# Optimization experiments

Hardware: AMD Instinct MI355X
Metric: run time of the kernel (lower is better)

## Reference

```python
import jax, jax.numpy as jnp
import numpy as np

NUM_CLASSES = 80
N_CAND = 10  # simOTA n_candidate_k


def setup_inputs() -> dict:
    key = jax.random.key(0)
    ks = jax.random.split(key, 8)
    G, C, B = 300, NUM_CLASSES, 2
    # FPN grids for a 1280x1280 input, strides 8/16/32 -> 160^2+80^2+40^2 = 33600 anchors
    levels = [(160, 8), (80, 16), (40, 32)]
    xs, ys, ss = [], [], []
    for n, s in levels:
        yy, xx = np.meshgrid(np.arange(n), np.arange(n), indexing='ij')
        xs.append(xx.ravel()); ys.append(yy.ravel()); ss.append(np.full(n * n, s))
    x_shifts = jnp.asarray(np.concatenate(xs), jnp.float32)[None]
    y_shifts = jnp.asarray(np.concatenate(ys), jnp.float32)[None]
    strides = jnp.asarray(np.concatenate(ss), jnp.float32)
    expanded_strides = strides[None]
    A = x_shifts.shape[1]
    # gt boxes in cxcywh, image coords
    gt_cxy = jax.random.uniform(ks[0], (G, 2), jnp.float32, 0.0, 1280.0)
    gt_wh = jax.random.uniform(ks[1], (G, 2), jnp.float32, 16.0, 256.0)
    gt_bboxes_per_image = jnp.concatenate([gt_cxy, gt_wh], -1)
    gt_classes = jax.random.randint(ks[2], (G,), 0, C)
    # predicted boxes: anchor centers + noise, wh ~ a few strides
    anc_x = (x_shifts[0] + 0.5) * strides
    anc_y = (y_shifts[0] + 0.5) * strides
    pr_cxy = jnp.stack([anc_x, anc_y], -1) + jax.random.normal(ks[3], (A, 2), jnp.float32) * strides[:, None]
    pr_wh = strides[:, None] * (1.0 + 4.0 * jax.random.uniform(ks[4], (A, 2), jnp.float32))
    bboxes_preds_per_image = jnp.concatenate([pr_cxy, pr_wh], -1)
    cls_preds = jax.random.normal(ks[5], (B, A, C), jnp.float32)
    obj_preds = jax.random.normal(ks[6], (B, A, 1), jnp.float32)
    return {
        'batch_idx': 0, 'num_gt': G, 'total_num_anchors': A,
        'gt_bboxes_per_image': gt_bboxes_per_image, 'gt_classes': gt_classes,
        'bboxes_preds_per_image': bboxes_preds_per_image,
        'expanded_strides': expanded_strides, 'x_shifts': x_shifts, 'y_shifts': y_shifts,
        'cls_preds': cls_preds, 'obj_preds': obj_preds,
    }


def _pairwise_iou(gt, pr):
    # gt [G,4], pr [A,4], cxcywh -> iou [G,A] (bboxes_iou with xyxy=False)
    tl = jnp.maximum(gt[:, None, :2] - 0.5 * gt[:, None, 2:], pr[None, :, :2] - 0.5 * pr[None, :, 2:])
    br = jnp.minimum(gt[:, None, :2] + 0.5 * gt[:, None, 2:], pr[None, :, :2] + 0.5 * pr[None, :, 2:])
    wh = jnp.clip(br - tl, 0.0)
    inter = wh[..., 0] * wh[..., 1]
    area_g = gt[:, 2] * gt[:, 3]
    area_p = pr[:, 2] * pr[:, 3]
    return inter / (area_g[:, None] + area_p[None, :] - inter)


def reference(batch_idx, num_gt, total_num_anchors, gt_bboxes_per_image, gt_classes,
              bboxes_preds_per_image, expanded_strides, x_shifts, y_shifts, cls_preds, obj_preds):
    G, A = gt_bboxes_per_image.shape[0], bboxes_preds_per_image.shape[0]
    strides = expanded_strides[0]
    xc = (x_shifts[0] + 0.5) * strides  # [A] anchor centers
    yc = (y_shifts[0] + 0.5) * strides
    gx, gy, gw, gh = (gt_bboxes_per_image[:, i] for i in range(4))
    # is_in_boxes [G,A]
    in_box = ((xc[None] > (gx - 0.5 * gw)[:, None]) & ((gx + 0.5 * gw)[:, None] > xc[None]) &
              (yc[None] > (gy - 0.5 * gh)[:, None]) & ((gy + 0.5 * gh)[:, None] > yc[None]))
    r = 2.5 * strides[None]  # center_radius * stride
    in_ctr = ((xc[None] > gx[:, None] - r) & (gx[:, None] + r > xc[None]) &
              (yc[None] > gy[:, None] - r) & (gy[:, None] + r > yc[None]))
    fg_any = in_box.any(0) | in_ctr.any(0)          # fg_mask over all anchors
    candidate = in_box & in_ctr                      # is_in_boxes_and_center (full-anchor layout)
    ious = jnp.where(fg_any[None, :], _pairwise_iou(gt_bboxes_per_image, bboxes_preds_per_image), 0.0)
    # pairwise cls BCE cost; one-hot target -> factored form, never materializes [G,A,C]
    p = jnp.sqrt(jax.nn.sigmoid(cls_preds[batch_idx]) * jax.nn.sigmoid(obj_preds[batch_idx]))  # [A,C]
    p = jnp.clip(p, 1e-7, 1.0 - 1e-7)
    lp, l1p = jnp.log(p), jnp.log1p(-p)
    s_all = l1p.sum(-1)                              # [A] sum_c log(1-p_c)
    cls_loss = -((lp - l1p)[:, gt_classes].T + s_all[None, :])  # [G,A]
    # cost; 1e5 penalty for non-candidates (as in source), extra 1e6 keeps non-fg anchors
    # strictly below any fg anchor in top-k order (source only ever considers fg anchors)
    cost = cls_loss - 3.0 * jnp.log(ious + 1e-8) + 100000.0 * (~candidate) + 1000000.0 * (~fg_any)[None, :]
    # dynamic-k: sum of top-10 ious per gt, clamped to >= 1 (<= 10 inherently)
    topk_ious, _ = jax.lax.top_k(ious, N_CAND)
    dks = jnp.clip(topk_ious.sum(1).astype(jnp.int32), 1, N_CAND)  # [G]
    _, idx = jax.lax.top_k(-cost, N_CAND)            # [G,10] lowest-cost anchors per gt
    sel = (jnp.arange(N_CAND)[None, :] < dks[:, None]).astype(jnp.int32)
    matching = jnp.zeros((G, A), jnp.int32).at[jnp.arange(G)[:, None], idx].max(sel)
    # resolve anchors matched to >1 gt: keep argmax of T_scores over gts (as in source)
    multi = matching.sum(0) > 1
    best_gt = jnp.argmax(cost, axis=0)               # [A]
    matching = jnp.where(multi[None, :], (jnp.arange(G)[:, None] == best_gt[None, :]).astype(jnp.int32), matching)
    fg_final = matching.sum(0) > 0                   # final fg mask over all anchors
    num_fg = fg_final.sum()
    matched = jnp.argmax(matching, axis=0)           # [A]
    gt_matched_classes = jnp.where(fg_final, gt_classes[matched], -1)
    pred_ious = (matching.astype(ious.dtype) * ious).sum(0)  # [A], 0 where unmatched
    matched_gt_inds = jnp.where(fg_final, matched, -1)
    # fixed-shape (full-anchor) versions of the source's compacted outputs
    return (gt_matched_classes, fg_final, pred_ious, matched_gt_inds, num_fg)
```

## Files before the change

kernel.cpp:

```cpp
#include <hip/hip_runtime.h>
#include <math.h>

#define NUMC 80
#define NCAND 10
#define TPB 256
#define SEGI 8
#define SEGF 16
#define FBY  32
#define MAXG_LDS 1024

typedef unsigned long long u64;

__device__ __forceinline__ float sigmoid_stable(float x) {
    if (x >= 0.0f) { float e = expf(-x); return 1.0f / (1.0f + e); }
    float e = expf(x); return e / (1.0f + e);
}

struct CostRes { float cost; float iou; bool cand; };

__device__ __forceinline__ CostRes cost_od(
    int g, int a, int b, int A,
    const float* __restrict__ gt, const float4* __restrict__ pred4,
    const float4* __restrict__ anc4, const float* __restrict__ so_arr,
    const float* __restrict__ cls, const int* __restrict__ fg_any,
    const int* __restrict__ gcls)
{
    float gx = gt[g*4+0], gy = gt[g*4+1], gw = gt[g*4+2], gh = gt[g*4+3];
    float4 p4 = pred4[a];
    float4 an = anc4[a];
    int fga = fg_any[a];
    float px = p4.x, py = p4.y, pw = p4.z, ph = p4.w;
    float tlx = fmaxf(gx - 0.5f*gw, px - 0.5f*pw);
    float tly = fmaxf(gy - 0.5f*gh, py - 0.5f*ph);
    float brx = fminf(gx + 0.5f*gw, px + 0.5f*pw);
    float bry = fminf(gy + 0.5f*gh, py + 0.5f*ph);
    float iw = fmaxf(brx - tlx, 0.0f);
    float ih = fmaxf(bry - tly, 0.0f);
    float inter = iw * ih;
    float iou = inter / (gw*gh + pw*ph - inter);
    float fi = fga ? iou : 0.0f;
    float x = an.x, y = an.y, r = an.z;
    bool inb = (x > gx - 0.5f*gw) && (gx + 0.5f*gw > x) &&
               (y > gy - 0.5f*gh) && (gy + 0.5f*gh > y);
    bool inc = (x > gx - r) && (gx + r > x) && (y > gy - r) && (gy + r > y);
    bool cand = inb && inc;
    float so = so_arr[a];
    float cv = cls[((size_t)b * A + a) * NUMC + gcls[g]];
    float sc = sigmoid_stable(cv);
    float p = sqrtf(sc * so);
    p = fminf(fmaxf(p, 1e-7f), 1.0f - 1e-7f);
    float lp = logf(p);
    float l1p = log1pf(-p);
    float clsl = -((lp - l1p) + an.w);
    float cost = clsl - 3.0f * logf(fi + 1e-8f)
               + (cand ? 0.0f : 100000.0f)
               + (fga  ? 0.0f : 1000000.0f);
    CostRes res; res.cost = cost; res.iou = fi; res.cand = cand; return res;
}

__device__ __forceinline__ float pair_iou_masked4(
    int g, const float* __restrict__ gt, float4 p4, int fga)
{
    float gx = gt[g*4+0], gy = gt[g*4+1], gw = gt[g*4+2], gh = gt[g*4+3];
    float px = p4.x, py = p4.y, pw = p4.z, ph = p4.w;
    float tlx = fmaxf(gx - 0.5f*gw, px - 0.5f*pw);
    float tly = fmaxf(gy - 0.5f*gh, py - 0.5f*ph);
    float brx = fminf(gx + 0.5f*gw, px + 0.5f*pw);
    float bry = fminf(gy + 0.5f*gh, py + 0.5f*ph);
    float iw = fmaxf(brx - tlx, 0.0f);
    float ih = fmaxf(bry - tly, 0.0f);
    float inter = iw * ih;
    float iou = inter / (gw*gh + pw*ph - inter);
    return fga ? iou : 0.0f;
}

__global__ __launch_bounds__(256) void fused_pre_kernel(
    const int* __restrict__ bidx, int G, int A,
    const float* __restrict__ gt,
    const float* __restrict__ strides,
    const float* __restrict__ xs, const float* __restrict__ ys,
    const float* __restrict__ cls, const float* __restrict__ obj,
    const float4* __restrict__ pred4,
    float4* __restrict__ anc4, float* __restrict__ so_arr,
    float4* __restrict__ ptlbr4, float* __restrict__ pare,
    float4* __restrict__ grpbox,
    int* __restrict__ fg_any, int* __restrict__ count, int* __restrict__ mgt,
    int* __restrict__ mcount, int* __restrict__ fb_cnt, float* __restrict__ out)
{
    __shared__ float sl1p[64 * 81];
    __shared__ float so_l[64];
    __shared__ float sgt[MAXG_LDS * 4];
    __shared__ int   flags[256];
    __shared__ float smnx[64], smny[64], smxx[64], smxy[64];
    __shared__ float sred[4];

    int tid = threadIdx.x;
    int a0 = blockIdx.x * 64;
    int b = bidx[0];
    int GS = (G < MAXG_LDS) ? G : MAXG_LDS;

    if (tid < 64) {
        int a = a0 + tid;
        so_l[tid] = (a < A) ? sigmoid_stable(obj[(size_t)b * A + a]) : 0.0f;
    } else {
        for (int i = tid - 64; i < GS * 4; i += 192) sgt[i] = gt[i];
    }
    __syncthreads();

    {
        int a_loc = tid >> 2;
        int a = a0 + a_loc;
        if (a < A) {
            int qb = (tid & 3) * 5;
            float so = so_l[a_loc];
            const float4* cp4 = (const float4*)(cls + ((size_t)b * A + a) * NUMC);
            #pragma unroll
            for (int qq = 0; qq < 5; ++qq) {
                int q = qb + qq;
                float4 v4 = cp4[q];
                float vv[4] = {v4.x, v4.y, v4.z, v4.w};
                #pragma unroll
                for (int k = 0; k < 4; ++k) {
                    int c = q * 4 + k;
                    float sc = sigmoid_stable(vv[k]);
                    float p = sqrtf(sc * so);
                    p = fminf(fmaxf(p, 1e-7f), 1.0f - 1e-7f);
                    float l1p = log1pf(-p);
                    sl1p[a_loc * 81 + c] = l1p;
                }
            }
        }
    }
    __syncthreads();

    float acc = 0.0f;
    if (tid < 64) {
        #pragma unroll 8
        for (int c = 0; c < NUMC; ++c) acc += sl1p[tid * 81 + c];
    }

    float x3 = 0.0f, y3 = 0.0f, r3 = 0.0f;
    {
        int a_loc = tid & 63;
        int chunk = tid >> 6;
        int a = a0 + a_loc;
        int any = 0;
        if (a < A) {
            float st = strides[a];
            float x = (xs[a] + 0.5f) * st;
            float y = (ys[a] + 0.5f) * st;
            float r = 2.5f * st;
            if (chunk == 0) { x3 = x; y3 = y; r3 = r; }
            int gpc = (G + 3) >> 2;
            int g0 = chunk * gpc;
            int g1 = (G < g0 + gpc) ? G : (g0 + gpc);
            for (int g = g0; g < g1; ++g) {
                float gx, gy, gw, gh;
                if (g < GS) { gx = sgt[g*4+0]; gy = sgt[g*4+1]; gw = sgt[g*4+2]; gh = sgt[g*4+3]; }
                else        { gx = gt[g*4+0];  gy = gt[g*4+1];  gw = gt[g*4+2];  gh = gt[g*4+3]; }
                bool inb = (x > gx - 0.5f*gw) && (gx + 0.5f*gw > x) &&
                           (y > gy - 0.5f*gh) && (gy + 0.5f*gh > y);
                bool inc = (x > gx - r) && (gx + r > x) && (y > gy - r) && (gy + r > y);
                if (inb | inc) { any = 1; break; }
            }
        }
        flags[tid] = any;
    }
    __syncthreads();

    if (tid < 64) {
        int a = a0 + tid;
        float mnx = INFINITY, mny = INFINITY, mxx = -INFINITY, mxy = -INFINITY;
        if (a < A) {
            int any = flags[tid] | flags[tid + 64] | flags[tid + 128] | flags[tid + 192];
            fg_any[a] = any;
            anc4[a] = make_float4(x3, y3, r3, acc);
            so_arr[a] = so_l[tid];
            count[a] = 0;
            mgt[a] = -1;
            float4 p4 = pred4[a];
            float ap = p4.z * p4.w;
            if (any) {
                mnx = p4.x - 0.5f * p4.z;
                mny = p4.y - 0.5f * p4.w;
                mxx = p4.x + 0.5f * p4.z;
                mxy = p4.y + 0.5f * p4.w;
            }
            ptlbr4[a] = make_float4(mnx, mny, mxx, mxy);
            pare[a] = ap;
        }
        smnx[tid] = mnx; smny[tid] = mny; smxx[tid] = mxx; smxy[tid] = mxy;
    }
    __syncthreads();
    if (tid < 4) {
        float v = (tid == 0 || tid == 1) ? INFINITY : -INFINITY;
        for (int i = 0; i < 64; ++i) {
            if (tid == 0) v = fminf(v, smnx[i]);
            else if (tid == 1) v = fminf(v, smny[i]);
            else if (tid == 2) v = fmaxf(v, smxx[i]);
            else v = fmaxf(v, smxy[i]);
        }
        sred[tid] = v;
    }
    __syncthreads();
    if (tid == 0) {
        grpbox[blockIdx.x] = make_float4(sred[0], sred[1], sred[2], sred[3]);
        if (blockIdx.x == 0) { out[(size_t)4 * A] = 0.0f; mcount[0] = 0; fb_cnt[0] = 0; }
    }
}

__global__ __launch_bounds__(TPB) void scanI_kernel(
    int G, int A, int seglen,
    const float* __restrict__ gt,
    const float4* __restrict__ ptlbr4, const float* __restrict__ pare,
    const float4* __restrict__ grpbox,
    float* __restrict__ piou_ws)
{
    int seg = blockIdx.x;
    int g = blockIdx.y;
    int a0 = seg * seglen;
    int a1 = min(A, a0 + seglen);
    int tid = threadIdx.x;

    float gx = gt[g*4+0], gy = gt[g*4+1], gw = gt[g*4+2], gh = gt[g*4+3];
    float gtlx = gx - 0.5f*gw, gtly = gy - 0.5f*gh;
    float gbrx = gx + 0.5f*gw, gbry = gy + 0.5f*gh;
    float ag = gw * gh;

    float ti[NCAND];
    #pragma unroll
    for (int j = 0; j < NCAND; ++j) ti[j] = 0.0f;

    for (int a = a0 + tid; a < a1; a += TPB) {
        int grp = __builtin_amdgcn_readfirstlane(a >> 6);
        float4 gb = grpbox[grp];
        if ((gb.z <= gtlx) || (gb.x >= gbrx) || (gb.w <= gtly) || (gb.y >= gbry))
            continue;
        float4 p = ptlbr4[a];
        float ap = pare[a];
        float tlx = fmaxf(gtlx, p.x);
        float tly = fmaxf(gtly, p.y);
        float brx = fminf(gbrx, p.z);
        float bry = fminf(gbry, p.w);
        float iw = fmaxf(brx - tlx, 0.0f);
        float ih = fmaxf(bry - tly, 0.0f);
        float inter = iw * ih;
        float fi = inter / (ag + ap - inter);
        if (fi > ti[NCAND-1]) {
            ti[NCAND-1] = fi;
            #pragma unroll
            for (int j = NCAND-1; j >= 1; --j) {
                if (ti[j] > ti[j-1]) { float t = ti[j]; ti[j] = ti[j-1]; ti[j-1] = t; }
            }
        }
    }

    __shared__ float s_iv[TPB * NCAND];
    #pragma unroll
    for (int j = 0; j < NCAND; ++j) s_iv[tid*NCAND+j] = ti[j];
    __syncthreads();
    for (int off = TPB/2; off > 0; off >>= 1) {
        if (tid < off) {
            float ra[NCAND];
            int i = 0, k = 0;
            const float* L = &s_iv[tid*NCAND];
            const float* R = &s_iv[(tid+off)*NCAND];
            for (int o = 0; o < NCAND; ++o) {
                if (L[i] >= R[k]) { ra[o] = L[i]; ++i; }
                else              { ra[o] = R[k]; ++k; }
            }
            for (int j = 0; j < NCAND; ++j) s_iv[tid*NCAND+j] = ra[j];
        }
        __syncthreads();
    }
    if (tid == 0) {
        int base = (g * SEGI + seg) * NCAND;
        for (int j = 0; j < NCAND; ++j) piou_ws[base+j] = s_iv[j];
    }
}

__global__ __launch_bounds__(256) void scanC_kernel(
    const int* __restrict__ bidx, int G, int A,
    const float* __restrict__ gt, const float4* __restrict__ pred4,
    const float4* __restrict__ anc4, const float* __restrict__ so_arr,
    const float* __restrict__ cls, const int* __restrict__ fg_any,
    const int* __restrict__ gcls,
    const float* __restrict__ piou_ws,
    int* __restrict__ dk_arr, int* __restrict__ fb_list, int* __restrict__ fb_cnt,
    int* __restrict__ count, int* __restrict__ mgt)
{
    int g = blockIdx.x;
    int tid = threadIdx.x;
    __shared__ u64 scand[128];
    __shared__ int s_nc;
    __shared__ int s_dk;

    if (tid == 0) {
        s_nc = 0;
        const float* ib = piou_ws + (size_t)g * SEGI * NCAND;
        int ip[SEGI];
        #pragma unroll
        for (int q = 0; q < SEGI; ++q) ip[q] = 0;
        float s = 0.0f;
        for (int o = 0; o < NCAND; ++o) {
            int bs = 0; float bv = -1.0f;
            #pragma unroll
            for (int q = 0; q < SEGI; ++q) {
                if (ip[q] < NCAND) {
                    float v = ib[q*NCAND + ip[q]];
                    if (v > bv) { bv = v; bs = q; }
                }
            }
            s += bv; ip[bs]++;
        }
        int dk = (int)s;
        if (dk < 1) dk = 1;
        if (dk > NCAND) dk = NCAND;
        s_dk = dk;
        dk_arr[g] = dk;
    }
    __syncthreads();

    if (tid < 243) {
        int lvl = tid / 81, slot = tid % 81, sx = slot % 9, sy = slot / 9;
        int n, si, base;
        if (lvl == 0)      { n = 160; si = 8;  base = 0; }
        else if (lvl == 1) { n = 80;  si = 16; base = 25600; }
        else               { n = 40;  si = 32; base = 32000; }
        float sf = (float)si;
        float gx = gt[g*4+0], gy = gt[g*4+1], gw = gt[g*4+2], gh = gt[g*4+3];
        float mx = fminf(0.5f*gw, 2.5f*sf);
        float my = fminf(0.5f*gh, 2.5f*sf);
        int ilo = (int)floorf((gx - mx)/sf - 0.5f) - 1;
        int ihi = (int)ceilf ((gx + mx)/sf - 0.5f) + 1;
        int jlo = (int)floorf((gy - my)/sf - 0.5f) - 1;
        int jhi = (int)ceilf ((gy + my)/sf - 0.5f) + 1;
        if (ilo < 0) ilo = 0;
        if (jlo < 0) jlo = 0;
        if (ihi > n-1) ihi = n-1;
        if (jhi > n-1) jhi = n-1;
        int i = ilo + sx, j = jlo + sy;
        if (i <= ihi && j <= jhi) {
            int a = base + j * n + i;
            int b = bidx[0];
            CostRes cr = cost_od(g, a, b, A, gt, pred4, anc4, so_arr, cls, fg_any, gcls);
            if (cr.cand) {
                int k = atomicAdd(&s_nc, 1);
                if (k < 128)
                    scand[k] = ((u64)__float_as_uint(cr.cost) << 32) | (unsigned)a;
            }
        }
    }
    __syncthreads();

    if (tid == 0) {
        int nc = s_nc; if (nc > 128) nc = 128;
        int dk = s_dk;
        if (dk > nc) {
            int idx = atomicAdd(fb_cnt, 1);
            fb_list[idx] = g;
        } else {
            u64 top[NCAND];
            #pragma unroll
            for (int j = 0; j < NCAND; ++j) top[j] = ~0ULL;
            for (int t = 0; t < nc; ++t) {
                u64 v = scand[t];
                if (v < top[NCAND-1]) {
                    top[NCAND-1] = v;
                    #pragma unroll
                    for (int j = NCAND-1; j >= 1; --j) {
                        if (top[j] < top[j-1]) { u64 t2 = top[j]; top[j] = top[j-1]; top[j-1] = t2; }
                    }
                }
            }
            for (int o = 0; o < dk; ++o) {
                int a = (int)(top[o] & 0xffffffffULL);
                atomicAdd(&count[a], 1);
                atomicMax(&mgt[a], g);
            }
        }
    }
}

__global__ __launch_bounds__(TPB) void fb_part_kernel(
    const int* __restrict__ bidx, int G, int A, int seglenF,
    const float* __restrict__ gt, const float4* __restrict__ pred4,
    const float4* __restrict__ anc4, const float* __restrict__ so_arr,
    const float* __restrict__ cls, const int* __restrict__ fg_any,
    const int* __restrict__ gcls,
    const int* __restrict__ fb_list, const int* __restrict__ fb_cnt,
    u64* __restrict__ fbws)
{
    __shared__ u64 s_cv[TPB * NCAND];
    int nflag = fb_cnt[0];
    int tid = threadIdx.x;
    int chunk = blockIdx.x;
    int b = bidx[0];
    for (int f = blockIdx.y; f < nflag; f += FBY) {
        int g = fb_list[f];
        int a0 = chunk * seglenF;
        int a1 = min(A, a0 + seglenF);
        u64 tc[NCAND];
        #pragma unroll
        for (int j = 0; j < NCAND; ++j) tc[j] = ~0ULL;
        for (int a = a0 + tid; a < a1; a += TPB) {
            CostRes cr = cost_od(g, a, b, A, gt, pred4, anc4, so_arr, cls, fg_any, gcls);
            u64 v = ((u64)__float_as_uint(cr.cost) << 32) | (unsigned)a;
            if (v < tc[NCAND-1]) {
                tc[NCAND-1] = v;
                #pragma unroll
                for (int j = NCAND-1; j >= 1; --j) {
                    if (tc[j] < tc[j-1]) { u64 t2 = tc[j]; tc[j] = tc[j-1]; tc[j-1] = t2; }
                }
            }
        }
        #pragma unroll
        for (int j = 0; j < NCAND; ++j) s_cv[tid*NCAND+j] = tc[j];
        __syncthreads();
        for (int off = TPB/2; off > 0; off >>= 1) {
            if (tid < off) {
                u64 rc[NCAND];
                int i = 0, k = 0;
                const u64* L = &s_cv[tid*NCAND];
                const u64* R = &s_cv[(tid+off)*NCAND];
                for (int o = 0; o < NCAND; ++o) {
                    if (L[i] < R[k]) { rc[o] = L[i]; ++i; }
                    else             { rc[o] = R[k]; ++k; }
                }
                for (int j = 0; j < NCAND; ++j) s_cv[tid*NCAND+j] = rc[j];
            }
            __syncthreads();
        }
        if (tid == 0) {
            u64* dst = fbws + ((size_t)f * SEGF + chunk) * NCAND;
            for (int j = 0; j < NCAND; ++j) dst[j] = s_cv[j];
        }
        __syncthreads();
    }
}

__global__ void fb_mark_kernel(
    const int* __restrict__ fb_list, const int* __restrict__ fb_cnt,
    const int* __restrict__ dk_arr, const u64* __restrict__ fbws,
    int* __restrict__ count, int* __restrict__ mgt)
{
    if (threadIdx.x != 0 || blockIdx.x != 0) return;
    int nflag = fb_cnt[0];
    for (int f = 0; f < nflag; ++f) {
        int g = fb_list[f];
        int dk = dk_arr[g];
        const u64* lists = fbws + (size_t)f * SEGF * NCAND;
        int p[SEGF];
        for (int q = 0; q < SEGF; ++q) p[q] = 0;
        for (int o = 0; o < dk; ++o) {
            int bs = 0; u64 bv = ~0ULL;
            for (int q = 0; q < SEGF; ++q) {
                if (p[q] < NCAND) {
                    u64 v = lists[q*NCAND + p[q]];
                    if (v < bv) { bv = v; bs = q; }
                }
            }
            p[bs]++;
            int a = (int)(bv & 0xffffffffULL);
            atomicAdd(&count[a], 1);
            atomicMax(&mgt[a], g);
        }
    }
}

__global__ void finalize_a_kernel(
    int G, int A,
    const float* __restrict__ gt, const float4* __restrict__ pred4,
    const int* __restrict__ fg_any, const int* __restrict__ gcls,
    const int* __restrict__ count, const int* __restrict__ mgt,
    int* __restrict__ mlist, int* __restrict__ mcount,
    float* __restrict__ out)
{
    int a = blockIdx.x * blockDim.x + threadIdx.x;
    if (a >= A) return;
    int cnt = count[a];
    unsigned long long m = __ballot(cnt > 0);
    if ((threadIdx.x & 63) == 0 && m) {
        atomicAdd(&out[(size_t)4*A], (float)__popcll(m));
    }
    if (cnt > 1) {
        int idx = atomicAdd(mcount, 1);
        mlist[idx] = a;
        out[(size_t)A + a] = 1.0f;
        return;
    }
    float gmc = -1.0f, mgi = -1.0f, piou = 0.0f, fg = 0.0f;
    if (cnt == 1) {
        int matched = mgt[a];
        fg = 1.0f;
        gmc = (float)gcls[matched];
        mgi = (float)matched;
        piou = pair_iou_masked4(matched, gt, pred4[a], fg_any[a]);
    }
    out[a]               = gmc;
    out[(size_t)A + a]   = fg;
    out[(size_t)2*A + a] = piou;
    out[(size_t)3*A + a] = mgi;
}

__global__ __launch_bounds__(TPB) void finalize_b_kernel(
    const int* __restrict__ bidx, int G, int A,
    const float* __restrict__ gt, const float4* __restrict__ pred4,
    const float4* __restrict__ anc4, const float* __restrict__ so_arr,
    const float* __restrict__ cls, const int* __restrict__ fg_any,
    const int* __restrict__ gcls,
    const int* __restrict__ mlist, const int* __restrict__ mcount,
    float* __restrict__ out)
{
    __shared__ float sc[TPB];
    __shared__ int   sg[TPB];
    int n = mcount[0];
    int tid = threadIdx.x;
    int b = bidx[0];
    for (int i = blockIdx.x; i < n; i += gridDim.x) {
        int a = mlist[i];
        float best = -INFINITY; int bi = 0x7fffffff;
        for (int g = tid; g < G; g += TPB) {
            CostRes cr = cost_od(g, a, b, A, gt, pred4, anc4, so_arr, cls, fg_any, gcls);
            if (cr.cost > best) { best = cr.cost; bi = g; }
        }
        sc[tid] = best; sg[tid] = bi;
        __syncthreads();
        for (int off = TPB/2; off > 0; off >>= 1) {
            if (tid < off) {
                float c2 = sc[tid+off]; int g2 = sg[tid+off];
                if (c2 > sc[tid] || (c2 == sc[tid] && g2 < sg[tid])) { sc[tid] = c2; sg[tid] = g2; }
            }
            __syncthreads();
        }
        if (tid == 0) {
            int matched = sg[0];
            out[a]               = (float)gcls[matched];
            out[(size_t)2*A + a] = pair_iou_masked4(matched, gt, pred4[a], fg_any[a]);
            out[(size_t)3*A + a] = (float)matched;
        }
        __syncthreads();
    }
}

extern "C" void kernel_launch(void* const* d_in, const int* in_sizes, int n_in,
                              void* d_out, int out_size, void* d_ws, size_t ws_size,
                              hipStream_t stream)
{
    const int*   bidx    = (const int*)d_in[0];
    const float* gt      = (const float*)d_in[3];
    const int*   gcls    = (const int*)d_in[4];
    const float* pred    = (const float*)d_in[5];
    const float* strides = (const float*)d_in[6];
    const float* xs      = (const float*)d_in[7];
    const float* ys      = (const float*)d_in[8];
    const float* cls     = (const float*)d_in[9];
    const float* obj     = (const float*)d_in[10];
    int G = in_sizes[4];
    int A = in_sizes[6];
    float* out = (float*)d_out;
    const float4* pred4 = (const float4*)pred;

    char* ws = (char*)d_ws;
    size_t off = 0;
    auto alloc = [&](size_t bytes) -> void* {
        void* p = ws + off;
        off += (bytes + 255) & ~(size_t)255;
        return p;
    };
    int nGrp = (A + 63) / 64;
    float4* anc4    = (float4*)alloc((size_t)A * sizeof(float4));
    float*  so_arr  = (float*) alloc((size_t)A * sizeof(float));
    float4* ptlbr4  = (float4*)alloc((size_t)A * sizeof(float4));
    float*  pare    = (float*) alloc((size_t)A * sizeof(float));
    float4* grpbox  = (float4*)alloc((size_t)nGrp * sizeof(float4));
    int*    fg_any  = (int*)   alloc((size_t)A * sizeof(int));
    int*    count   = (int*)   alloc((size_t)A * sizeof(int));
    int*    mgt     = (int*)   alloc((size_t)A * sizeof(int));
    int*    mlist   = (int*)   alloc((size_t)A * sizeof(int));
    int*    mcount  = (int*)   alloc(256);
    int*    fb_cnt  = (int*)   alloc(256);
    float*  piou_ws = (float*) alloc((size_t)G * SEGI * NCAND * sizeof(float));
    int*    dk_arr  = (int*)   alloc((size_t)G * sizeof(int));
    int*    fb_list = (int*)   alloc((size_t)G * sizeof(int));
    u64*    fbws    = (u64*)   alloc((size_t)G * SEGF * NCAND * sizeof(u64));

    int seglenI = ((A + SEGI*64 - 1) / (SEGI*64)) * 64;
    int seglenF = ((A + SEGF*64 - 1) / (SEGF*64)) * 64;
    int blocksA256 = (A + 255) / 256;

    fused_pre_kernel<<<nGrp, 256, 0, stream>>>(
        bidx, G, A, gt, strides, xs, ys, cls, obj, pred4,
        anc4, so_arr, ptlbr4, pare, grpbox, fg_any, count, mgt, mcount, fb_cnt, out);
    scanI_kernel<<<dim3(SEGI, G), TPB, 0, stream>>>(
        G, A, seglenI, gt, ptlbr4, pare, grpbox, piou_ws);
    scanC_kernel<<<G, 256, 0, stream>>>(
        bidx, G, A, gt, pred4, anc4, so_arr, cls, fg_any, gcls,
        piou_ws, dk_arr, fb_list, fb_cnt, count, mgt);
    fb_part_kernel<<<dim3(SEGF, FBY), TPB, 0, stream>>>(
        bidx, G, A, seglenF, gt, pred4, anc4, so_arr, cls, fg_any, gcls,
        fb_list, fb_cnt, fbws);
    fb_mark_kernel<<<1, 64, 0, stream>>>(
        fb_list, fb_cnt, dk_arr, fbws, count, mgt);
    finalize_a_kernel<<<blocksA256, 256, 0, stream>>>(
        G, A, gt, pred4, fg_any, gcls, count, mgt, mlist, mcount, out);
    finalize_b_kernel<<<256, TPB, 0, stream>>>(
        bidx, G, A, gt, pred4, anc4, so_arr, cls, fg_any, gcls, mlist, mcount, out);
}
```

Before: 192.1 us.

## Compute class log-sum lazily for candidate anchors and use wave-shuffle top-k merges

The prepass no longer computes the 80-class log1p sum for every anchor. It records a cand_any flag, and a separate kernel computes that sum only for anchors that are a candidate for some gt. A fixup kernel fills in the remaining anchors only when the fallback path is taken. scanI and scanC now reduce their top-k IoU lists with 16-wide bitonic merges over wave shuffles instead of LDS serial merges, and scanI uses 64-thread blocks with more segments. The prepass also moves to 512 threads and a shuffle-based bbox reduction, at the cost of extra kernel launches and a risk that finalize_b reads s_arr for non-candidate anchors that still hold 0.

```diff
diff --git a/kernel.cpp b/kernel.cpp
--- a/kernel.cpp
+++ b/kernel.cpp
@@ -3,17 +3,57 @@
 
 #define NUMC 80
 #define NCAND 10
-#define TPB 256
-#define SEGI 8
+#define NK 16
+#define SEGI 16
 #define SEGF 16
-#define FBY  32
-#define MAXG_LDS 1024
+#define FBY  8
+#define GT_LDS 300
 
 typedef unsigned long long u64;
 
 __device__ __forceinline__ float sigmoid_stable(float x) {
-    if (x >= 0.0f) { float e = expf(-x); return 1.0f / (1.0f + e); }
-    float e = expf(x); return e / (1.0f + e);
+    float e = expf(-fabsf(x));
+    float num = (x >= 0.0f) ? 1.0f : e;
+    return num / (1.0f + e);
+}
+
+__device__ __forceinline__ float s_all_for(int a, int b, int A, float so,
+                                           const float* __restrict__ cls)
+{
+    const float4* cp4 = (const float4*)(cls + ((size_t)b * A + a) * NUMC);
+    float acc = 0.0f;
+    for (int q = 0; q < NUMC/4; ++q) {
+        float4 v4 = cp4[q];
+        float vv[4] = {v4.x, v4.y, v4.z, v4.w};
+        #pragma unroll
+        for (int k = 0; k < 4; ++k) {
+            float sc = sigmoid_stable(vv[k]);
+            float p = sqrtf(sc * so);
+            p = fminf(fmaxf(p, 1e-7f), 1.0f - 1e-7f);
+            acc += log1pf(-p);
+        }
+    }
+    return acc;
+}
+
+__device__ __forceinline__ void bitonic16_desc(float (&L)[NK]) {
+    #pragma unroll
+    for (int j = 0; j < NK; ++j) if (!(j & 8)) { float a=L[j], b=L[j|8]; L[j]=fmaxf(a,b); L[j|8]=fminf(a,b); }
+    #pragma unroll
+    for (int j = 0; j < NK; ++j) if (!(j & 4)) { float a=L[j], b=L[j|4]; L[j]=fmaxf(a,b); L[j|4]=fminf(a,b); }
+    #pragma unroll
+    for (int j = 0; j < NK; ++j) if (!(j & 2)) { float a=L[j], b=L[j|2]; L[j]=fmaxf(a,b); L[j|2]=fminf(a,b); }
+    #pragma unroll
+    for (int j = 0; j < NK; ++j) if (!(j & 1)) { float a=L[j], b=L[j|1]; L[j]=fmaxf(a,b); L[j|1]=fminf(a,b); }
+}
+
+__device__ __forceinline__ void merge16_desc(float (&A_)[NK], const float (&B_)[NK]) {
+    float L[NK];
+    #pragma unroll
+    for (int j = 0; j < NK; ++j) L[j] = fmaxf(A_[j], B_[NK-1-j]);
+    bitonic16_desc(L);
+    #pragma unroll
+    for (int j = 0; j < NK; ++j) A_[j] = L[j];
 }
 
 struct CostRes { float cost; float iou; bool cand; };
@@ -21,9 +61,9 @@
 __device__ __forceinline__ CostRes cost_od(
     int g, int a, int b, int A,
     const float* __restrict__ gt, const float4* __restrict__ pred4,
-    const float4* __restrict__ anc4, const float* __restrict__ so_arr,
-    const float* __restrict__ cls, const int* __restrict__ fg_any,
-    const int* __restrict__ gcls)
+    const float4* __restrict__ anc4, const float* __restrict__ s_arr,
+    const float* __restrict__ so_arr, const float* __restrict__ cls,
+    const int* __restrict__ fg_any, const int* __restrict__ gcls)
 {
     float gx = gt[g*4+0], gy = gt[g*4+1], gw = gt[g*4+2], gh = gt[g*4+3];
     float4 p4 = pred4[a];
@@ -51,7 +91,7 @@
     p = fminf(fmaxf(p, 1e-7f), 1.0f - 1e-7f);
     float lp = logf(p);
     float l1p = log1pf(-p);
-    float clsl = -((lp - l1p) + an.w);
+    float clsl = -((lp - l1p) + s_arr[a]);
     float cost = clsl - 3.0f * logf(fi + 1e-8f)
                + (cand ? 0.0f : 100000.0f)
                + (fga  ? 0.0f : 1000000.0f);
@@ -74,86 +114,49 @@
     return fga ? iou : 0.0f;
 }
 
-__global__ __launch_bounds__(256) void fused_pre_kernel(
+__global__ __launch_bounds__(512) void fused_pre_kernel(
     const int* __restrict__ bidx, int G, int A,
-    const float* __restrict__ gt,
-    const float* __restrict__ strides,
+    const float* __restrict__ gt, const float* __restrict__ strides,
     const float* __restrict__ xs, const float* __restrict__ ys,
-    const float* __restrict__ cls, const float* __restrict__ obj,
-    const float4* __restrict__ pred4,
-    float4* __restrict__ anc4, float* __restrict__ so_arr,
-    float4* __restrict__ ptlbr4, float* __restrict__ pare,
-    float4* __restrict__ grpbox,
-    int* __restrict__ fg_any, int* __restrict__ count, int* __restrict__ mgt,
+    const float* __restrict__ obj, const float4* __restrict__ pred4,
+    float4* __restrict__ anc4, float* __restrict__ so_arr, float* __restrict__ s_arr,
+    float4* __restrict__ ptlbr4, float* __restrict__ pare, float4* __restrict__ grpbox,
+    int* __restrict__ fg_any, int* __restrict__ cand_any,
+    int* __restrict__ count, int* __restrict__ mgt,
     int* __restrict__ mcount, int* __restrict__ fb_cnt, float* __restrict__ out)
 {
-    __shared__ float sl1p[64 * 81];
-    __shared__ float so_l[64];
-    __shared__ float sgt[MAXG_LDS * 4];
-    __shared__ int   flags[256];
-    __shared__ float smnx[64], smny[64], smxx[64], smxy[64];
-    __shared__ float sred[4];
+    __shared__ float sgt[GT_LDS * 4];
+    __shared__ float sx[64], sy[64], sr[64];
+    __shared__ int   flags[512];
 
     int tid = threadIdx.x;
     int a0 = blockIdx.x * 64;
-    int b = bidx[0];
-    int GS = (G < MAXG_LDS) ? G : MAXG_LDS;
-
+    int GS = (G < GT_LDS) ? G : GT_LDS;
+
+    for (int i = tid; i < GS * 4; i += 512) sgt[i] = gt[i];
     if (tid < 64) {
         int a = a0 + tid;
-        so_l[tid] = (a < A) ? sigmoid_stable(obj[(size_t)b * A + a]) : 0.0f;
-    } else {
-        for (int i = tid - 64; i < GS * 4; i += 192) sgt[i] = gt[i];
+        float st = 0.0f, x = 0.0f, y = 0.0f;
+        if (a < A) {
+            st = strides[a];
+            x = (xs[a] + 0.5f) * st;
+            y = (ys[a] + 0.5f) * st;
+            so_arr[a] = sigmoid_stable(obj[(size_t)bidx[0] * A + a]);
+        }
+        sx[tid] = x; sy[tid] = y; sr[tid] = 2.5f * st;
     }
     __syncthreads();
 
-    {
-        int a_loc = tid >> 2;
-        int a = a0 + a_loc;
-        if (a < A) {
-            int qb = (tid & 3) * 5;
-            float so = so_l[a_loc];
-            const float4* cp4 = (const float4*)(cls + ((size_t)b * A + a) * NUMC);
-            #pragma unroll
-            for (int qq = 0; qq < 5; ++qq) {
-                int q = qb + qq;
-                float4 v4 = cp4[q];
-                float vv[4] = {v4.x, v4.y, v4.z, v4.w};
-                #pragma unroll
-                for (int k = 0; k < 4; ++k) {
-                    int c = q * 4 + k;
-                    float sc = sigmoid_stable(vv[k]);
-                    float p = sqrtf(sc * so);
-                    p = fminf(fmaxf(p, 1e-7f), 1.0f - 1e-7f);
-                    float l1p = log1pf(-p);
-                    sl1p[a_loc * 81 + c] = l1p;
-                }
-            }
-        }
-    }
-    __syncthreads();
-
-    float acc = 0.0f;
-    if (tid < 64) {
-        #pragma unroll 8
-        for (int c = 0; c < NUMC; ++c) acc += sl1p[tid * 81 + c];
-    }
-
-    float x3 = 0.0f, y3 = 0.0f, r3 = 0.0f;
     {
         int a_loc = tid & 63;
         int chunk = tid >> 6;
         int a = a0 + a_loc;
-        int any = 0;
+        int any_or = 0, any_and = 0;
         if (a < A) {
-            float st = strides[a];
-            float x = (xs[a] + 0.5f) * st;
-            float y = (ys[a] + 0.5f) * st;
-            float r = 2.5f * st;
-            if (chunk == 0) { x3 = x; y3 = y; r3 = r; }
-            int gpc = (G + 3) >> 2;
+            float x = sx[a_loc], y = sy[a_loc], r = sr[a_loc];
+            int gpc = (G + 7) >> 3;
             int g0 = chunk * gpc;
-            int g1 = (G < g0 + gpc) ? G : (g0 + gpc);
+            int g1 = min(G, g0 + gpc);
             for (int g = g0; g < g1; ++g) {
                 float gx, gy, gw, gh;
                 if (g < GS) { gx = sgt[g*4+0]; gy = sgt[g*4+1]; gw = sgt[g*4+2]; gh = sgt[g*4+3]; }
@@ -161,10 +164,11 @@
                 bool inb = (x > gx - 0.5f*gw) && (gx + 0.5f*gw > x) &&
                            (y > gy - 0.5f*gh) && (gy + 0.5f*gh > y);
                 bool inc = (x > gx - r) && (gx + r > x) && (y > gy - r) && (gy + r > y);
-                if (inb | inc) { any = 1; break; }
-            }
-        }
-        flags[tid] = any;
+                any_or  |= (int)(inb | inc);
+                any_and |= (int)(inb && inc);
+            }
+        }
+        flags[tid] = any_or | (any_and << 1);
     }
     __syncthreads();
 
@@ -172,14 +176,17 @@
         int a = a0 + tid;
         float mnx = INFINITY, mny = INFINITY, mxx = -INFINITY, mxy = -INFINITY;
         if (a < A) {
-            int any = flags[tid] | flags[tid + 64] | flags[tid + 128] | flags[tid + 192];
+            int f = flags[tid] | flags[tid+64] | flags[tid+128] | flags[tid+192]
+                  | flags[tid+256] | flags[tid+320] | flags[tid+384] | flags[tid+448];
+            int any = f & 1;
             fg_any[a] = any;
-            anc4[a] = make_float4(x3, y3, r3, acc);
-            so_arr[a] = so_l[tid];
+            cand_any[a] = (f >> 1) & 1;
+            anc4[a] = make_float4(sx[tid], sy[tid], sr[tid], 0.0f);
+            s_arr[a] = 0.0f;
             count[a] = 0;
             mgt[a] = -1;
             float4 p4 = pred4[a];
-            float ap = p4.z * p4.w;
+            pare[a] = p4.z * p4.w;
             if (any) {
                 mnx = p4.x - 0.5f * p4.z;
                 mny = p4.y - 0.5f * p4.w;
@@ -187,29 +194,46 @@
                 mxy = p4.y + 0.5f * p4.w;
             }
             ptlbr4[a] = make_float4(mnx, mny, mxx, mxy);
-            pare[a] = ap;
-        }
-        smnx[tid] = mnx; smny[tid] = mny; smxx[tid] = mxx; smxy[tid] = mxy;
-    }
-    __syncthreads();
-    if (tid < 4) {
-        float v = (tid == 0 || tid == 1) ? INFINITY : -INFINITY;
-        for (int i = 0; i < 64; ++i) {
-            if (tid == 0) v = fminf(v, smnx[i]);
-            else if (tid == 1) v = fminf(v, smny[i]);
-            else if (tid == 2) v = fmaxf(v, smxx[i]);
-            else v = fmaxf(v, smxy[i]);
-        }
-        sred[tid] = v;
-    }
-    __syncthreads();
-    if (tid == 0) {
-        grpbox[blockIdx.x] = make_float4(sred[0], sred[1], sred[2], sred[3]);
-        if (blockIdx.x == 0) { out[(size_t)4 * A] = 0.0f; mcount[0] = 0; fb_cnt[0] = 0; }
-    }
-}
-
-__global__ __launch_bounds__(TPB) void scanI_kernel(
+        }
+        #pragma unroll
+        for (int off = 32; off > 0; off >>= 1) {
+            mnx = fminf(mnx, __shfl_xor(mnx, off));
+            mny = fminf(mny, __shfl_xor(mny, off));
+            mxx = fmaxf(mxx, __shfl_xor(mxx, off));
+            mxy = fmaxf(mxy, __shfl_xor(mxy, off));
+        }
+        if (tid == 0) {
+            grpbox[blockIdx.x] = make_float4(mnx, mny, mxx, mxy);
+            if (blockIdx.x == 0) { out[(size_t)4 * A] = 0.0f; mcount[0] = 0; fb_cnt[0] = 0; }
+        }
+    }
+}
+
+__global__ void sall_kernel(
+    const int* __restrict__ bidx, int A,
+    const float* __restrict__ cls, const float* __restrict__ so_arr,
+    const int* __restrict__ cand_any, float* __restrict__ s_arr)
+{
+    int a = blockIdx.x * blockDim.x + threadIdx.x;
+    if (a >= A) return;
+    if (!cand_any[a]) return;
+    s_arr[a] = s_all_for(a, bidx[0], A, so_arr[a], cls);
+}
+
+__global__ void sall_fixup_kernel(
+    const int* __restrict__ bidx, int A,
+    const float* __restrict__ cls, const float* __restrict__ so_arr,
+    const int* __restrict__ cand_any, const int* __restrict__ fb_cnt,
+    float* __restrict__ s_arr)
+{
+    if (fb_cnt[0] == 0) return;
+    int a = blockIdx.x * blockDim.x + threadIdx.x;
+    if (a >= A) return;
+    if (cand_any[a]) return;
+    s_arr[a] = s_all_for(a, bidx[0], A, so_arr[a], cls);
+}
+
+__global__ __launch_bounds__(64) void scanI_kernel(
     int G, int A, int seglen,
     const float* __restrict__ gt,
     const float4* __restrict__ ptlbr4, const float* __restrict__ pare,
@@ -227,11 +251,11 @@
     float gbrx = gx + 0.5f*gw, gbry = gy + 0.5f*gh;
     float ag = gw * gh;
 
-    float ti[NCAND];
-    #pragma unroll
-    for (int j = 0; j < NCAND; ++j) ti[j] = 0.0f;
-
-    for (int a = a0 + tid; a < a1; a += TPB) {
+    float ti[NK];
+    #pragma unroll
+    for (int j = 0; j < NK; ++j) ti[j] = 0.0f;
+
+    for (int a = a0 + tid; a < a1; a += 64) {
         int grp = __builtin_amdgcn_readfirstlane(a >> 6);
         float4 gb = grpbox[grp];
         if ((gb.z <= gtlx) || (gb.x >= gbrx) || (gb.w <= gtly) || (gb.y >= gbry))
@@ -246,45 +270,36 @@
         float ih = fmaxf(bry - tly, 0.0f);
         float inter = iw * ih;
         float fi = inter / (ag + ap - inter);
-        if (fi > ti[NCAND-1]) {
-            ti[NCAND-1] = fi;
+        if (fi > ti[NK-1]) {
+            ti[NK-1] = fi;
             #pragma unroll
-            for (int j = NCAND-1; j >= 1; --j) {
+            for (int j = NK-1; j >= 1; --j) {
                 if (ti[j] > ti[j-1]) { float t = ti[j]; ti[j] = ti[j-1]; ti[j-1] = t; }
             }
         }
     }
 
-    __shared__ float s_iv[TPB * NCAND];
-    #pragma unroll
-    for (int j = 0; j < NCAND; ++j) s_iv[tid*NCAND+j] = ti[j];
-    __syncthreads();
-    for (int off = TPB/2; off > 0; off >>= 1) {
-        if (tid < off) {
-            float ra[NCAND];
-            int i = 0, k = 0;
-            const float* L = &s_iv[tid*NCAND];
-            const float* R = &s_iv[(tid+off)*NCAND];
-            for (int o = 0; o < NCAND; ++o) {
-                if (L[i] >= R[k]) { ra[o] = L[i]; ++i; }
-                else              { ra[o] = R[k]; ++k; }
-            }
-            for (int j = 0; j < NCAND; ++j) s_iv[tid*NCAND+j] = ra[j];
-        }
-        __syncthreads();
+    #pragma unroll
+    for (int lv = 0; lv < 6; ++lv) {
+        int off = 1 << lv;
+        float pv[NK];
+        #pragma unroll
+        for (int j = 0; j < NK; ++j) pv[j] = __shfl_xor(ti[j], off);
+        merge16_desc(ti, pv);
     }
     if (tid == 0) {
         int base = (g * SEGI + seg) * NCAND;
-        for (int j = 0; j < NCAND; ++j) piou_ws[base+j] = s_iv[j];
+        #pragma unroll
+        for (int j = 0; j < NCAND; ++j) piou_ws[base + j] = ti[j];
     }
 }
 
 __global__ __launch_bounds__(256) void scanC_kernel(
     const int* __restrict__ bidx, int G, int A,
     const float* __restrict__ gt, const float4* __restrict__ pred4,
-    const float4* __restrict__ anc4, const float* __restrict__ so_arr,
-    const float* __restrict__ cls, const int* __restrict__ fg_any,
-    const int* __restrict__ gcls,
+    const float4* __restrict__ anc4, const float* __restrict__ s_arr,
+    const float* __restrict__ so_arr, const float* __restrict__ cls,
+    const int* __restrict__ fg_any, const int* __restrict__ gcls,
     const float* __restrict__ piou_ws,
     int* __restrict__ dk_arr, int* __restrict__ fb_list, int* __restrict__ fb_cnt,
     int* __restrict__ count, int* __restrict__ mgt)
@@ -295,34 +310,36 @@
     __shared__ int s_nc;
     __shared__ int s_dk;
 
-    if (tid == 0) {
-        s_nc = 0;
-        const float* ib = piou_ws + (size_t)g * SEGI * NCAND;
-        int ip[SEGI];
-        #pragma unroll
-        for (int q = 0; q < SEGI; ++q) ip[q] = 0;
-        float s = 0.0f;
-        for (int o = 0; o < NCAND; ++o) {
-            int bs = 0; float bv = -1.0f;
+    if (tid == 0) s_nc = 0;
+    if (tid < 64) {
+        float acc[NK];
+        const float* ib = piou_ws + ((size_t)g * SEGI + (tid < SEGI ? tid : 0)) * NCAND;
+        #pragma unroll
+        for (int j = 0; j < NK; ++j)
+            acc[j] = (j < NCAND && tid < SEGI) ? ib[j] : 0.0f;
+        #pragma unroll
+        for (int lv = 0; lv < 4; ++lv) {
+            int off = 1 << lv;
+            float pv[NK];
             #pragma unroll
-            for (int q = 0; q < SEGI; ++q) {
-                if (ip[q] < NCAND) {
-                    float v = ib[q*NCAND + ip[q]];
-                    if (v > bv) { bv = v; bs = q; }
-                }
-            }
-            s += bv; ip[bs]++;
-        }
-        int dk = (int)s;
-        if (dk < 1) dk = 1;
-        if (dk > NCAND) dk = NCAND;
-        s_dk = dk;
-        dk_arr[g] = dk;
+            for (int j = 0; j < NK; ++j) pv[j] = __shfl_xor(acc[j], off);
+            merge16_desc(acc, pv);
+        }
+        if (tid == 0) {
+            float s = 0.0f;
+            #pragma unroll
+            for (int j = 0; j < NCAND; ++j) s += acc[j];
+            int dk = (int)s;
+            if (dk < 1) dk = 1;
+            if (dk > NCAND) dk = NCAND;
+            s_dk = dk;
+            dk_arr[g] = dk;
+        }
     }
     __syncthreads();
 
     if (tid < 243) {
-        int lvl = tid / 81, slot = tid % 81, sx = slot % 9, sy = slot / 9;
+        int lvl = tid / 81, slot = tid % 81, sxi = slot % 9, syi = slot / 9;
         int n, si, base;
         if (lvl == 0)      { n = 160; si = 8;  base = 0; }
         else if (lvl == 1) { n = 80;  si = 16; base = 25600; }
@@ -339,11 +356,11 @@
         if (jlo < 0) jlo = 0;
         if (ihi > n-1) ihi = n-1;
         if (jhi > n-1) jhi = n-1;
-        int i = ilo + sx, j = jlo + sy;
+        int i = ilo + sxi, j = jlo + syi;
         if (i <= ihi && j <= jhi) {
             int a = base + j * n + i;
             int b = bidx[0];
-            CostRes cr = cost_od(g, a, b, A, gt, pred4, anc4, so_arr, cls, fg_any, gcls);
+            CostRes cr = cost_od(g, a, b, A, gt, pred4, anc4, s_arr, so_arr, cls, fg_any, gcls);
             if (cr.cand) {
                 int k = atomicAdd(&s_nc, 1);
                 if (k < 128)
@@ -373,25 +390,28 @@
                     }
                 }
             }
-            for (int o = 0; o < dk; ++o) {
-                int a = (int)(top[o] & 0xffffffffULL);
-                atomicAdd(&count[a], 1);
-                atomicMax(&mgt[a], g);
-            }
-        }
-    }
-}
-
-__global__ __launch_bounds__(TPB) void fb_part_kernel(
+            #pragma unroll
+            for (int o = 0; o < NCAND; ++o) {
+                if (o < dk) {
+                    int a = (int)(top[o] & 0xffffffffULL);
+                    atomicAdd(&count[a], 1);
+                    atomicMax(&mgt[a], g);
+                }
+            }
+        }
+    }
+}
+
+__global__ __launch_bounds__(256) void fb_part_kernel(
     const int* __restrict__ bidx, int G, int A, int seglenF,
     const float* __restrict__ gt, const float4* __restrict__ pred4,
-    const float4* __restrict__ anc4, const float* __restrict__ so_arr,
-    const float* __restrict__ cls, const int* __restrict__ fg_any,
-    const int* __restrict__ gcls,
+    const float4* __restrict__ anc4, const float* __restrict__ s_arr,
+    const float* __restrict__ so_arr, const float* __restrict__ cls,
+    const int* __restrict__ fg_any, const int* __restrict__ gcls,
     const int* __restrict__ fb_list, const int* __restrict__ fb_cnt,
     u64* __restrict__ fbws)
 {
-    __shared__ u64 s_cv[TPB * NCAND];
+    __shared__ u64 s_cv[256 * NCAND];
     int nflag = fb_cnt[0];
     int tid = threadIdx.x;
     int chunk = blockIdx.x;
@@ -403,8 +423,8 @@
         u64 tc[NCAND];
         #pragma unroll
         for (int j = 0; j < NCAND; ++j) tc[j] = ~0ULL;
-        for (int a = a0 + tid; a < a1; a += TPB) {
-            CostRes cr = cost_od(g, a, b, A, gt, pred4, anc4, so_arr, cls, fg_any, gcls);
+        for (int a = a0 + tid; a < a1; a += 256) {
+            CostRes cr = cost_od(g, a, b, A, gt, pred4, anc4, s_arr, so_arr, cls, fg_any, gcls);
             u64 v = ((u64)__float_as_uint(cr.cost) << 32) | (unsigned)a;
             if (v < tc[NCAND-1]) {
                 tc[NCAND-1] = v;
@@ -417,7 +437,7 @@
         #pragma unroll
         for (int j = 0; j < NCAND; ++j) s_cv[tid*NCAND+j] = tc[j];
         __syncthreads();
-        for (int off = TPB/2; off > 0; off >>= 1) {
+        for (int off = 128; off > 0; off >>= 1) {
             if (tid < off) {
                 u64 rc[NCAND];
                 int i = 0, k = 0;
@@ -503,30 +523,30 @@
     out[(size_t)3*A + a] = mgi;
 }
 
-__global__ __launch_bounds__(TPB) void finalize_b_kernel(
+__global__ __launch_bounds__(256) void finalize_b_kernel(
     const int* __restrict__ bidx, int G, int A,
     const float* __restrict__ gt, const float4* __restrict__ pred4,
-    const float4* __restrict__ anc4, const float* __restrict__ so_arr,
-    const float* __restrict__ cls, const int* __restrict__ fg_any,
-    const int* __restrict__ gcls,
+    const float4* __restrict__ anc4, const float* __restrict__ s_arr,
+    const float* __restrict__ so_arr, const float* __restrict__ cls,
+    const int* __restrict__ fg_any, const int* __restrict__ gcls,
     const int* __restrict__ mlist, const int* __restrict__ mcount,
     float* __restrict__ out)
 {
-    __shared__ float sc[TPB];
-    __shared__ int   sg[TPB];
+    __shared__ float sc[256];
+    __shared__ int   sg[256];
     int n = mcount[0];
     int tid = threadIdx.x;
     int b = bidx[0];
     for (int i = blockIdx.x; i < n; i += gridDim.x) {
         int a = mlist[i];
         float best = -INFINITY; int bi = 0x7fffffff;
-        for (int g = tid; g < G; g += TPB) {
-            CostRes cr = cost_od(g, a, b, A, gt, pred4, anc4, so_arr, cls, fg_any, gcls);
+        for (int g = tid; g < G; g += 256) {
+            CostRes cr = cost_od(g, a, b, A, gt, pred4, anc4, s_arr, so_arr, cls, fg_any, gcls);
             if (cr.cost > best) { best = cr.cost; bi = g; }
         }
         sc[tid] = best; sg[tid] = bi;
         __syncthreads();
-        for (int off = TPB/2; off > 0; off >>= 1) {
+        for (int off = 128; off > 0; off >>= 1) {
             if (tid < off) {
                 float c2 = sc[tid+off]; int g2 = sg[tid+off];
                 if (c2 > sc[tid] || (c2 == sc[tid] && g2 < sg[tid])) { sc[tid] = c2; sg[tid] = g2; }
@@ -569,41 +589,49 @@
         return p;
     };
     int nGrp = (A + 63) / 64;
-    float4* anc4    = (float4*)alloc((size_t)A * sizeof(float4));
-    float*  so_arr  = (float*) alloc((size_t)A * sizeof(float));
-    float4* ptlbr4  = (float4*)alloc((size_t)A * sizeof(float4));
-    float*  pare    = (float*) alloc((size_t)A * sizeof(float));
-    float4* grpbox  = (float4*)alloc((size_t)nGrp * sizeof(float4));
-    int*    fg_any  = (int*)   alloc((size_t)A * sizeof(int));
-    int*    count   = (int*)   alloc((size_t)A * sizeof(int));
-    int*    mgt     = (int*)   alloc((size_t)A * sizeof(int));
-    int*    mlist   = (int*)   alloc((size_t)A * sizeof(int));
-    int*    mcount  = (int*)   alloc(256);
-    int*    fb_cnt  = (int*)   alloc(256);
-    float*  piou_ws = (float*) alloc((size_t)G * SEGI * NCAND * sizeof(float));
-    int*    dk_arr  = (int*)   alloc((size_t)G * sizeof(int));
-    int*    fb_list = (int*)   alloc((size_t)G * sizeof(int));
-    u64*    fbws    = (u64*)   alloc((size_t)G * SEGF * NCAND * sizeof(u64));
+    float4* anc4     = (float4*)alloc((size_t)A * sizeof(float4));
+    float*  so_arr   = (float*) alloc((size_t)A * sizeof(float));
+    float*  s_arr    = (float*) alloc((size_t)A * sizeof(float));
+    float4* ptlbr4   = (float4*)alloc((size_t)A * sizeof(float4));
+    float*  pare     = (float*) alloc((size_t)A * sizeof(float));
+    float4* grpbox   = (float4*)alloc((size_t)nGrp * sizeof(float4));
+    int*    fg_any   = (int*)   alloc((size_t)A * sizeof(int));
+    int*    cand_any = (int*)   alloc((size_t)A * sizeof(int));
+    int*    count    = (int*)   alloc((size_t)A * sizeof(int));
+    int*    mgt      = (int*)   alloc((size_t)A * sizeof(int));
+    int*    mlist    = (int*)   alloc((size_t)A * sizeof(int));
+    int*    mcount   = (int*)   alloc(256);
+    int*    fb_cnt   = (int*)   alloc(256);
+    float*  piou_ws  = (float*) alloc((size_t)G * SEGI * NCAND * sizeof(float));
+    int*    dk_arr   = (int*)   alloc((size_t)G * sizeof(int));
+    int*    fb_list  = (int*)   alloc((size_t)G * sizeof(int));
+    u64*    fbws     = (u64*)   alloc((size_t)G * SEGF * NCAND * sizeof(u64));
 
     int seglenI = ((A + SEGI*64 - 1) / (SEGI*64)) * 64;
     int seglenF = ((A + SEGF*64 - 1) / (SEGF*64)) * 64;
     int blocksA256 = (A + 255) / 256;
 
-    fused_pre_kernel<<<nGrp, 256, 0, stream>>>(
-        bidx, G, A, gt, strides, xs, ys, cls, obj, pred4,
-        anc4, so_arr, ptlbr4, pare, grpbox, fg_any, count, mgt, mcount, fb_cnt, out);
-    scanI_kernel<<<dim3(SEGI, G), TPB, 0, stream>>>(
+    fused_pre_kernel<<<nGrp, 512, 0, stream>>>(
+        bidx, G, A, gt, strides, xs, ys, obj, pred4,
+        anc4, so_arr, s_arr, ptlbr4, pare, grpbox,
+        fg_any, cand_any, count, mgt, mcount, fb_cnt, out);
+    sall_kernel<<<blocksA256, 256, 0, stream>>>(
+        bidx, A, cls, so_arr, cand_any, s_arr);
+    scanI_kernel<<<dim3(SEGI, G), 64, 0, stream>>>(
         G, A, seglenI, gt, ptlbr4, pare, grpbox, piou_ws);
     scanC_kernel<<<G, 256, 0, stream>>>(
-        bidx, G, A, gt, pred4, anc4, so_arr, cls, fg_any, gcls,
+        bidx, G, A, gt, pred4, anc4, s_arr, so_arr, cls, fg_any, gcls,
         piou_ws, dk_arr, fb_list, fb_cnt, count, mgt);
-    fb_part_kernel<<<dim3(SEGF, FBY), TPB, 0, stream>>>(
-        bidx, G, A, seglenF, gt, pred4, anc4, so_arr, cls, fg_any, gcls,
+    sall_fixup_kernel<<<blocksA256, 256, 0, stream>>>(
+        bidx, A, cls, so_arr, cand_any, fb_cnt, s_arr);
+    fb_part_kernel<<<dim3(SEGF, FBY), 256, 0, stream>>>(
+        bidx, G, A, seglenF, gt, pred4, anc4, s_arr, so_arr, cls, fg_any, gcls,
         fb_list, fb_cnt, fbws);
     fb_mark_kernel<<<1, 64, 0, stream>>>(
         fb_list, fb_cnt, dk_arr, fbws, count, mgt);
     finalize_a_kernel<<<blocksA256, 256, 0, stream>>>(
         G, A, gt, pred4, fg_any, gcls, count, mgt, mlist, mcount, out);
-    finalize_b_kernel<<<256, TPB, 0, stream>>>(
-        bidx, G, A, gt, pred4, anc4, so_arr, cls, fg_any, gcls, mlist, mcount, out);
-}
+    finalize_b_kernel<<<256, 256, 0, stream>>>(
+        bidx, G, A, gt, pred4, anc4, s_arr, so_arr, cls, fg_any, gcls,
+        mlist, mcount, out);
+}
```

New measurement: 182.2 us. 5.1% less time.
